# Optimization experiments

Measured on AMD Instinct MI355X. Metric: run time of the kernel, lower is better.

The kernel has to match this reference:

```python
import jax, jax.numpy as jnp
import numpy as np

B, LQ, LK, D = 4, 2048, 2048, 1024
H = 16  # num_heads == num_kv_heads (only runnable config of the source module)
HD = D // H  # 64


def setup_inputs() -> dict:
    key = jax.random.key(0)
    ks = jax.random.split(key, 4)
    std = 0.02
    return {
        "x": jax.random.normal(ks[0], (B, LQ, D), dtype=jnp.float32),
        "text_input": jax.random.normal(ks[1], (B, LK, D), dtype=jnp.float32),
        "Wq": jax.random.normal(ks[2], (D, D), dtype=jnp.float32) * std,
        "bq": jnp.zeros((D,), dtype=jnp.float32),
        "Wkv": jax.random.normal(ks[3], (D, 2 * D), dtype=jnp.float32) * std,
        "bkv": jnp.zeros((2 * D,), dtype=jnp.float32),
    }


def reference(x, text_input, Wq, bq, Wkv, bkv):
    b, lq, d = x.shape
    lk = text_input.shape[1]
    # projections
    Q = x @ Wq + bq                       # [b, lq, d]
    KV = text_input @ Wkv + bkv           # [b, lk, 2d]
    K, V = jnp.split(KV, 2, axis=-1)      # [b, lk, d] each
    # split heads (num_kv_heads == num_heads, so repeat_interleave is identity)
    Q = Q.reshape(b, lq, H, HD)
    K = K.reshape(b, lk, H, HD)
    V = V.reshape(b, lk, H, HD)
    # scaled dot-product attention
    scale = 1.0 / jnp.sqrt(jnp.asarray(HD, dtype=Q.dtype))
    scores = jnp.einsum("bqhd,bkhd->bhqk", Q, K) * scale  # [b, H, lq, lk]
    attn = jax.nn.softmax(scores, axis=-1)
    out = jnp.einsum("bhqk,bkhd->bqhd", attn, V)          # [b, lq, H, HD]
    # dropout p=0.0 (eval) -> identity
    return out.reshape(b, lq, d)
```

## Files before the change

### kernel.cpp

```cpp
#include <hip/hip_runtime.h>
#include <hip/hip_bf16.h>


typedef unsigned short u16;
typedef unsigned int u32;

typedef __attribute__((ext_vector_type(8))) __bf16 bf16x8;
typedef __attribute__((ext_vector_type(2))) _Float16 f16x2;
typedef __attribute__((ext_vector_type(8))) _Float16 f16x8;
typedef __attribute__((ext_vector_type(4))) float f32x4;
typedef __attribute__((ext_vector_type(4))) float f4;
typedef __attribute__((ext_vector_type(4))) unsigned short u16x4;

#define DEVI __device__ __forceinline__

DEVI u16 f2b(float f) {
  u32 u = __float_as_uint(f);
  return (u16)((u + 0x7fffu + ((u >> 16) & 1u)) >> 16);
}

DEVI u16 f2h(float f) {
  _Float16 h = (_Float16)f;
  return __builtin_bit_cast(u16, h);
}

DEVI f16x2 pk_f16(float a, float b) {
  return __builtin_bit_cast(f16x2, __builtin_amdgcn_cvt_pkrtz(a, b));
}

DEVI void gld_lds16(void* lds, const void* g) {
  __builtin_amdgcn_global_load_lds(
      (const __attribute__((address_space(1))) u32*)g,
      (__attribute__((address_space(3))) u32*)lds, 16, 0, 0);
}

__global__ __launch_bounds__(256) void k_prep(
    const float* __restrict__ x, const float* __restrict__ text,
    const float* __restrict__ Wq, const float* __restrict__ Wkv,
    u16* __restrict__ XB, u16* __restrict__ TB,
    u16* __restrict__ WQT, u16* __restrict__ WKVT) {
  __shared__ float tile[32][33];
  const int bid = blockIdx.x, tid = threadIdx.x;
  if (bid < 4096) {
    const float* in = (bid < 2048) ? x : text;
    u16* out = (bid < 2048) ? XB : TB;
    const int cb = (bid < 2048) ? bid : bid - 2048;
#pragma unroll
    for (int it = 0; it < 4; it++) {
      int i = cb * 256 + tid + it * 524288;
      f4 v = ((const f4*)in)[i];
      u16x4 o;
      o.x = f2b(v.x); o.y = f2b(v.y); o.z = f2b(v.z); o.w = f2b(v.w);
      ((u16x4*)out)[i] = o;
    }
  } else {
    const float* in;
    u16* out;
    int N, bx, by;
    if (bid < 5120) {
      int b2 = bid - 4096; in = Wq; out = WQT; N = 1024; bx = b2 & 31; by = b2 >> 5;
    } else {
      int b2 = bid - 5120; in = Wkv; out = WKVT; N = 2048; bx = b2 & 63; by = b2 >> 6;
    }
    const int K = 1024;
    const int n0 = bx * 32, k0 = by * 32;
    const int tx = tid & 31, ty = tid >> 5;
#pragma unroll
    for (int j = 0; j < 32; j += 8)
      tile[ty + j][tx] = in[(size_t)(k0 + ty + j) * N + n0 + tx];
    __syncthreads();
#pragma unroll
    for (int j = 0; j < 32; j += 8)
      out[(size_t)(n0 + ty + j) * K + k0 + tx] = f2b(tile[tx][ty + j]);
  }
}

__global__ __launch_bounds__(256) void k_gemm(
    const u16* __restrict__ XB, const u16* __restrict__ TB,
    const u16* __restrict__ WQT, const u16* __restrict__ WKVT,
    const float* __restrict__ bq, const float* __restrict__ bkv,
    u16* __restrict__ QG, u16* __restrict__ KG, u16* __restrict__ VG) {
  __shared__ alignas(16) char As[2][8192];
  __shared__ alignas(16) char Bs[2][8192];
  const int bid = blockIdx.x;
  const int tid = threadIdx.x;
  const int w = tid >> 6, l = tid & 63;
  const int wr = w >> 1, wc = w & 1;

  const bool isQ = bid < 512;
  int nb, mb;
  const u16 *Aptr, *Bptr;
  const float* bias;
  if (isQ) {
    nb = bid & 7; mb = bid >> 3; Aptr = XB; Bptr = WQT; bias = bq;
  } else {
    int b2 = bid - 512; nb = b2 & 15; mb = b2 >> 4; Aptr = TB; Bptr = WKVT; bias = bkv;
  }
  const int m0 = mb << 7, n0 = nb << 7;

  u32 soff[2], doff[2];
#pragma unroll
  for (int i = 0; i < 2; i++) {
    u32 o = (u32)(i * 4096 + tid * 16);
    u32 row = o >> 6;
    soff[i] = row * 2048 + ((o & 63) ^ ((row & 3) << 4));
    doff[i] = o;
  }
  const char* Aorig = (const char*)Aptr + (size_t)m0 * 2048;
  const char* Borig = (const char*)Bptr + (size_t)n0 * 2048;

  f32x4 acc[4][4];
#pragma unroll
  for (int i = 0; i < 4; i++)
#pragma unroll
    for (int j = 0; j < 4; j++) acc[i][j] = (f32x4){0.f, 0.f, 0.f, 0.f};

  const u32 co = (u32)(((l >> 4) ^ (l & 3)) << 4);
  const u32 arow = (u32)(wr * 64 + (l & 15)) * 64;
  const u32 brow = (u32)(wc * 64 + (l & 15)) * 64;

#pragma unroll
  for (int i = 0; i < 2; i++) {
    gld_lds16(&As[0][doff[i]], Aorig + soff[i]);
    gld_lds16(&Bs[0][doff[i]], Borig + soff[i]);
  }
  __syncthreads();
  int buf = 0;
  for (int kt = 0; kt < 32; kt++) {
    if (kt < 31) {
#pragma unroll
      for (int i = 0; i < 2; i++) {
        gld_lds16(&As[buf ^ 1][doff[i]], Aorig + (u32)(kt + 1) * 64 + soff[i]);
        gld_lds16(&Bs[buf ^ 1][doff[i]], Borig + (u32)(kt + 1) * 64 + soff[i]);
      }
    }
    bf16x8 af[4], bfr[4];
#pragma unroll
    for (int t = 0; t < 4; t++) {
      af[t] = *(const bf16x8*)&As[buf][arow + (u32)t * 1024 + co];
      bfr[t] = *(const bf16x8*)&Bs[buf][brow + (u32)t * 1024 + co];
    }
#pragma unroll
    for (int i = 0; i < 4; i++)
#pragma unroll
      for (int j = 0; j < 4; j++)
        acc[i][j] = __builtin_amdgcn_mfma_f32_16x16x32_bf16(af[i], bfr[j], acc[i][j], 0, 0, 0);
    __syncthreads();
    buf ^= 1;
  }

#pragma unroll
  for (int i = 0; i < 4; i++) {
    const int mbase = m0 + wr * 64 + i * 16 + ((l >> 4) << 2);
    const int bb = mbase >> 11;
    const int mrow = mbase & 2047;
#pragma unroll
    for (int j = 0; j < 4; j++) {
      const int n = n0 + wc * 64 + j * 16 + (l & 15);
      const float bv = bias[n];
      if (isQ) {
        const int h = n >> 6, hd = n & 63;
        u16* dst = QG + ((((size_t)bb * 16 + h) * 2048 + mrow) << 6) + hd;
#pragma unroll
        for (int r = 0; r < 4; r++)
          dst[(size_t)r << 6] = f2b((acc[i][j][r] + bv) * 0.18033688011112042f);
      } else if (n < 1024) {
        const int h = n >> 6, d = n & 63;
        char* base = (char*)KG + ((((size_t)bb * 16 + h) * 2048 + mrow) << 7);
#pragma unroll
        for (int r = 0; r < 4; r++) {
          u32 off = (u32)r * 128 + (((u32)d * 2) ^ (((u32)(mrow + r) & 7) << 4));
          *(u16*)(base + off) = f2b(acc[i][j][r] + bv);
        }
      } else {
        const int nn = n - 1024;
        const int h = nn >> 6, hd = nn & 63;
        u16x4 pk;
        pk.x = f2h(acc[i][j][0] + bv);
        pk.y = f2h(acc[i][j][1] + bv);
        pk.z = f2h(acc[i][j][2] + bv);
        pk.w = f2h(acc[i][j][3] + bv);
        char* base = (char*)VG + (((size_t)bb * 16 + h) << 18);
        u32 off = ((u32)(mrow >> 6) << 13) + (((u32)(mrow >> 5) & 1) << 12) +
                  ((u32)(hd >> 4) << 10) + (((u32)(mrow >> 2) & 3) << 8) +
                  ((u32)(hd & 15) << 4) + (((u32)(mrow >> 4) & 1) << 3);
        *(u16x4*)(base + off) = pk;
      }
    }
  }
}

__global__ __launch_bounds__(256) void k_attn(
    const u16* __restrict__ QG, const u16* __restrict__ KG, const u16* __restrict__ VG,
    float* __restrict__ out) {
  __shared__ alignas(16) char Ks[2][8192];
  __shared__ alignas(16) char Vs[2][8192];
  const int tid = threadIdx.x, w = tid >> 6, l = tid & 63;
  const int g = l >> 4, q = l & 15;
  const int bid = blockIdx.x;
  const int orig = (bid & 7) * 128 + (bid >> 3);
  const int qt = orig & 15;
  const int hh = (orig >> 4) & 15;
  const int b = orig >> 8;
  const size_t bh = (size_t)b * 16 + hh;

  const int qrowA = qt * 128 + w * 16 + q;
  const int qrowB = qrowA + 64;

  const u16* QpA = QG + ((bh * 2048 + (size_t)qrowA) << 6) + (g << 3);
  const u16* QpB = QG + ((bh * 2048 + (size_t)qrowB) << 6) + (g << 3);
  const bf16x8 qf0a = *(const bf16x8*)QpA;
  const bf16x8 qf1a = *(const bf16x8*)(QpA + 32);
  const bf16x8 qf0b = *(const bf16x8*)QpB;
  const bf16x8 qf1b = *(const bf16x8*)(QpB + 32);

  const char* Kbase = (const char*)KG + (bh << 18);
  const char* Vbase = (const char*)VG + (bh << 18);

  f32x4 lsA = (f32x4){0.f, 0.f, 0.f, 0.f};
  f32x4 lsB = (f32x4){0.f, 0.f, 0.f, 0.f};
  f32x4 oa[4], ob4[4];
#pragma unroll
  for (int c = 0; c < 4; c++) {
    oa[c] = (f32x4){0.f, 0.f, 0.f, 0.f};
    ob4[c] = (f32x4){0.f, 0.f, 0.f, 0.f};
  }
  f16x8 ones8;
#pragma unroll
  for (int e = 0; e < 8; e++) ones8[e] = (_Float16)1.0f;

  gld_lds16(&Ks[0][tid * 16], Kbase + tid * 16);
  gld_lds16(&Ks[0][4096 + tid * 16], Kbase + 4096 + tid * 16);
  gld_lds16(&Vs[0][tid * 16], Vbase + tid * 16);
  gld_lds16(&Vs[0][4096 + tid * 16], Vbase + 4096 + tid * 16);
  __syncthreads();

  const u32 ksw = ((u32)(l & 7)) << 4;
  const u32 kro = ((u32)q) << 7;
  const u32 kin = ((u32)g) << 4;

  auto body = [&](int BUF, int kb) {
    if (kb < 31) {
      const char* kp = Kbase + (size_t)(kb + 1) * 8192 + tid * 16;
      const char* vp = Vbase + (size_t)(kb + 1) * 8192 + tid * 16;
      gld_lds16(&Ks[BUF ^ 1][tid * 16], kp);
      gld_lds16(&Ks[BUF ^ 1][4096 + tid * 16], kp + 4096);
      gld_lds16(&Vs[BUF ^ 1][tid * 16], vp);
      gld_lds16(&Vs[BUF ^ 1][4096 + tid * 16], vp + 4096);
    }
    f32x4 sa[4], sb[4];
    __builtin_amdgcn_s_setprio(1);
#pragma unroll
    for (int t = 0; t < 4; t++) {
      const char* kr = &Ks[BUF][kro + (u32)t * 2048];
      bf16x8 kf0 = *(const bf16x8*)(kr + (kin ^ ksw));
      bf16x8 kf1 = *(const bf16x8*)(kr + ((kin + 64) ^ ksw));
      f32x4 z = (f32x4){0.f, 0.f, 0.f, 0.f};
      sa[t] = __builtin_amdgcn_mfma_f32_16x16x32_bf16(kf0, qf0a, z, 0, 0, 0);
      sa[t] = __builtin_amdgcn_mfma_f32_16x16x32_bf16(kf1, qf1a, sa[t], 0, 0, 0);
      sb[t] = __builtin_amdgcn_mfma_f32_16x16x32_bf16(kf0, qf0b, z, 0, 0, 0);
      sb[t] = __builtin_amdgcn_mfma_f32_16x16x32_bf16(kf1, qf1b, sb[t], 0, 0, 0);
    }
    __builtin_amdgcn_s_setprio(0);

    float pA[4][4], pB[4][4];
#pragma unroll
    for (int t = 0; t < 4; t++)
#pragma unroll
      for (int r = 0; r < 4; r++) {
        pA[t][r] = __builtin_amdgcn_exp2f(sa[t][r]);
        pB[t][r] = __builtin_amdgcn_exp2f(sb[t][r]);
      }

    __builtin_amdgcn_s_setprio(1);
#pragma unroll
    for (int u = 0; u < 2; u++) {
      f16x2 a0 = pk_f16(pA[2 * u][0], pA[2 * u][1]);
      f16x2 a1 = pk_f16(pA[2 * u][2], pA[2 * u][3]);
      f16x2 a2 = pk_f16(pA[2 * u + 1][0], pA[2 * u + 1][1]);
      f16x2 a3 = pk_f16(pA[2 * u + 1][2], pA[2 * u + 1][3]);
      f16x8 pfa;
      pfa[0] = a0.x; pfa[1] = a0.y; pfa[2] = a1.x; pfa[3] = a1.y;
      pfa[4] = a2.x; pfa[5] = a2.y; pfa[6] = a3.x; pfa[7] = a3.y;
      f16x2 b0 = pk_f16(pB[2 * u][0], pB[2 * u][1]);
      f16x2 b1 = pk_f16(pB[2 * u][2], pB[2 * u][3]);
      f16x2 b2 = pk_f16(pB[2 * u + 1][0], pB[2 * u + 1][1]);
      f16x2 b3 = pk_f16(pB[2 * u + 1][2], pB[2 * u + 1][3]);
      f16x8 pfb;
      pfb[0] = b0.x; pfb[1] = b0.y; pfb[2] = b1.x; pfb[3] = b1.y;
      pfb[4] = b2.x; pfb[5] = b2.y; pfb[6] = b3.x; pfb[7] = b3.y;
      lsA = __builtin_amdgcn_mfma_f32_16x16x32_f16(ones8, pfa, lsA, 0, 0, 0);
      lsB = __builtin_amdgcn_mfma_f32_16x16x32_f16(ones8, pfb, lsB, 0, 0, 0);
#pragma unroll
      for (int c = 0; c < 4; c++) {
        f16x8 vf = *(const f16x8*)&Vs[BUF][(u32)u * 4096 + (u32)c * 1024 + (u32)l * 16];
        oa[c] = __builtin_amdgcn_mfma_f32_16x16x32_f16(vf, pfa, oa[c], 0, 0, 0);
        ob4[c] = __builtin_amdgcn_mfma_f32_16x16x32_f16(vf, pfb, ob4[c], 0, 0, 0);
      }
    }
    __builtin_amdgcn_s_setprio(0);
    __syncthreads();
  };

  for (int kb2 = 0; kb2 < 16; kb2++) {
    body(0, 2 * kb2);
    body(1, 2 * kb2 + 1);
  }

  const float invA = 1.0f / lsA.x;
  const float invB = 1.0f / lsB.x;
  float* obA = out + ((size_t)b * 2048 + (size_t)qrowA) * 1024 + hh * 64;
  float* obB = out + ((size_t)b * 2048 + (size_t)qrowB) * 1024 + hh * 64;
#pragma unroll
  for (int c = 0; c < 4; c++) {
    f32x4 va = oa[c] * invA;
    f32x4 vb2 = ob4[c] * invB;
    *(f32x4*)(obA + c * 16 + g * 4) = va;
    *(f32x4*)(obB + c * 16 + g * 4) = vb2;
  }
}

extern "C" void kernel_launch(void* const* d_in, const int* in_sizes, int n_in,
                              void* d_out, int out_size, void* d_ws, size_t ws_size,
                              hipStream_t stream) {
  const float* x = (const float*)d_in[0];
  const float* text = (const float*)d_in[1];
  const float* Wq = (const float*)d_in[2];
  const float* bq = (const float*)d_in[3];
  const float* Wkv = (const float*)d_in[4];
  const float* bkv = (const float*)d_in[5];
  float* out = (float*)d_out;
  char* ws = (char*)d_ws;

  const size_t MiB = 1u << 20;
  u16* XB = (u16*)(ws + 0 * MiB);
  u16* TB = (u16*)(ws + 16 * MiB);
  u16* WQT = (u16*)(ws + 32 * MiB);
  u16* WKVT = (u16*)(ws + 34 * MiB);
  u16* QG = (u16*)(ws + 38 * MiB);
  u16* KG = (u16*)(ws + 54 * MiB);
  u16* VG = (u16*)(ws + 70 * MiB);

  k_prep<<<7168, 256, 0, stream>>>(x, text, Wq, Wkv, XB, TB, WQT, WKVT);
  k_gemm<<<1536, 256, 0, stream>>>(XB, TB, WQT, WKVT, bq, bkv, QG, KG, VG);
  k_attn<<<1024, 256, 0, stream>>>(QG, KG, VG, out);
}
```

Baseline: 181.7 us.

## Use 32x32 MFMA in projection GEMM and VALU row sums in attention

The projection GEMM moves from 16x16x32 to 32x32x16 bf16 MFMA tiles, with new LDS fragment indexing and an epilogue that matches the 32x32 accumulator layout. This cuts LDS fragment loads per MFMA and raises operand reuse. In attention, the softmax denominator is no longer computed with a ones-vector MFMA. Each lane now sums its exp values in fp32 registers and the partial sums are reduced with cross-lane shuffles at the end, which frees the matrix pipe but adds VALU adds and keeps the denominator in fp32 instead of the fp16-rounded values.

```diff
diff --git a/kernel.cpp b/kernel.cpp
--- a/kernel.cpp
+++ b/kernel.cpp
@@ -9,8 +9,10 @@
 typedef __attribute__((ext_vector_type(2))) _Float16 f16x2;
 typedef __attribute__((ext_vector_type(8))) _Float16 f16x8;
 typedef __attribute__((ext_vector_type(4))) float f32x4;
+typedef __attribute__((ext_vector_type(16))) float f32x16;
 typedef __attribute__((ext_vector_type(4))) float f4;
 typedef __attribute__((ext_vector_type(4))) unsigned short u16x4;
+typedef __attribute__((ext_vector_type(4))) unsigned int u32x4;
 
 #define DEVI __device__ __forceinline__
 
@@ -24,8 +26,8 @@
   return __builtin_bit_cast(u16, h);
 }
 
-DEVI f16x2 pk_f16(float a, float b) {
-  return __builtin_bit_cast(f16x2, __builtin_amdgcn_cvt_pkrtz(a, b));
+DEVI u32 pk_f16u(float a, float b) {
+  return __builtin_bit_cast(u32, __builtin_amdgcn_cvt_pkrtz(a, b));
 }
 
 DEVI void gld_lds16(void* lds, const void* g) {
@@ -109,15 +111,18 @@
   const char* Aorig = (const char*)Aptr + (size_t)m0 * 2048;
   const char* Borig = (const char*)Bptr + (size_t)n0 * 2048;
 
-  f32x4 acc[4][4];
-#pragma unroll
-  for (int i = 0; i < 4; i++)
-#pragma unroll
-    for (int j = 0; j < 4; j++) acc[i][j] = (f32x4){0.f, 0.f, 0.f, 0.f};
-
-  const u32 co = (u32)(((l >> 4) ^ (l & 3)) << 4);
-  const u32 arow = (u32)(wr * 64 + (l & 15)) * 64;
-  const u32 brow = (u32)(wc * 64 + (l & 15)) * 64;
+  f32x16 acc[2][2];
+#pragma unroll
+  for (int i = 0; i < 2; i++)
+#pragma unroll
+    for (int j = 0; j < 2; j++)
+#pragma unroll
+      for (int e = 0; e < 16; e++) acc[i][j][e] = 0.f;
+
+  const u32 x3 = (u32)(l & 3);
+  const u32 hi5 = (u32)(l >> 5);
+  const u32 arow0 = (u32)(wr * 64 + (l & 31)) * 64;
+  const u32 brow0 = (u32)(wc * 64 + (l & 31)) * 64;
 
 #pragma unroll
   for (int i = 0; i < 2; i++) {
@@ -134,60 +139,70 @@
         gld_lds16(&Bs[buf ^ 1][doff[i]], Borig + (u32)(kt + 1) * 64 + soff[i]);
       }
     }
-    bf16x8 af[4], bfr[4];
-#pragma unroll
-    for (int t = 0; t < 4; t++) {
-      af[t] = *(const bf16x8*)&As[buf][arow + (u32)t * 1024 + co];
-      bfr[t] = *(const bf16x8*)&Bs[buf][brow + (u32)t * 1024 + co];
-    }
-#pragma unroll
-    for (int i = 0; i < 4; i++)
-#pragma unroll
-      for (int j = 0; j < 4; j++)
-        acc[i][j] = __builtin_amdgcn_mfma_f32_16x16x32_bf16(af[i], bfr[j], acc[i][j], 0, 0, 0);
+    bf16x8 af[2][2], bfr[2][2];
+#pragma unroll
+    for (int i = 0; i < 2; i++)
+#pragma unroll
+      for (int h = 0; h < 2; h++) {
+        const u32 co = (((u32)(2 * h) + hi5) ^ x3) << 4;
+        af[i][h] = *(const bf16x8*)&As[buf][arow0 + (u32)i * 2048 + co];
+        bfr[i][h] = *(const bf16x8*)&Bs[buf][brow0 + (u32)i * 2048 + co];
+      }
+#pragma unroll
+    for (int i = 0; i < 2; i++)
+#pragma unroll
+      for (int j = 0; j < 2; j++)
+#pragma unroll
+        for (int h = 0; h < 2; h++)
+          acc[i][j] = __builtin_amdgcn_mfma_f32_32x32x16_bf16(af[i][h], bfr[j][h], acc[i][j], 0, 0, 0);
     __syncthreads();
     buf ^= 1;
   }
 
 #pragma unroll
-  for (int i = 0; i < 4; i++) {
-    const int mbase = m0 + wr * 64 + i * 16 + ((l >> 4) << 2);
-    const int bb = mbase >> 11;
-    const int mrow = mbase & 2047;
-#pragma unroll
-    for (int j = 0; j < 4; j++) {
-      const int n = n0 + wc * 64 + j * 16 + (l & 15);
+  for (int i = 0; i < 2; i++)
+#pragma unroll
+    for (int j = 0; j < 2; j++) {
+      const int n = n0 + wc * 64 + j * 32 + (l & 31);
       const float bv = bias[n];
-      if (isQ) {
-        const int h = n >> 6, hd = n & 63;
-        u16* dst = QG + ((((size_t)bb * 16 + h) * 2048 + mrow) << 6) + hd;
-#pragma unroll
-        for (int r = 0; r < 4; r++)
-          dst[(size_t)r << 6] = f2b((acc[i][j][r] + bv) * 0.18033688011112042f);
-      } else if (n < 1024) {
-        const int h = n >> 6, d = n & 63;
-        char* base = (char*)KG + ((((size_t)bb * 16 + h) * 2048 + mrow) << 7);
-#pragma unroll
-        for (int r = 0; r < 4; r++) {
-          u32 off = (u32)r * 128 + (((u32)d * 2) ^ (((u32)(mrow + r) & 7) << 4));
-          *(u16*)(base + off) = f2b(acc[i][j][r] + bv);
+#pragma unroll
+      for (int rg = 0; rg < 4; rg++) {
+        const int mbase = m0 + wr * 64 + i * 32 + rg * 8 + ((l >> 5) << 2);
+        const int bb = mbase >> 11;
+        const int mrow = mbase & 2047;
+        float a0 = acc[i][j][rg * 4 + 0] + bv;
+        float a1 = acc[i][j][rg * 4 + 1] + bv;
+        float a2 = acc[i][j][rg * 4 + 2] + bv;
+        float a3 = acc[i][j][rg * 4 + 3] + bv;
+        if (isQ) {
+          const int h = n >> 6, hd = n & 63;
+          u16* dst = QG + ((((size_t)bb * 16 + h) * 2048 + mrow) << 6) + hd;
+          dst[0] = f2b(a0 * 0.18033688011112042f);
+          dst[64] = f2b(a1 * 0.18033688011112042f);
+          dst[128] = f2b(a2 * 0.18033688011112042f);
+          dst[192] = f2b(a3 * 0.18033688011112042f);
+        } else if (n < 1024) {
+          const int h = n >> 6, d = n & 63;
+          char* base = (char*)KG + ((((size_t)bb * 16 + h) * 2048 + mrow) << 7);
+          float av[4] = {a0, a1, a2, a3};
+#pragma unroll
+          for (int r = 0; r < 4; r++) {
+            u32 off = (u32)r * 128 + (((u32)d * 2) ^ (((u32)(mrow + r) & 7) << 4));
+            *(u16*)(base + off) = f2b(av[r]);
+          }
+        } else {
+          const int nn = n - 1024;
+          const int h = nn >> 6, hd = nn & 63;
+          u16x4 pk;
+          pk.x = f2h(a0); pk.y = f2h(a1); pk.z = f2h(a2); pk.w = f2h(a3);
+          char* base = (char*)VG + (((size_t)bb * 16 + h) << 18);
+          u32 off = ((u32)(mrow >> 6) << 13) + (((u32)(mrow >> 5) & 1) << 12) +
+                    ((u32)(hd >> 4) << 10) + (((u32)(mrow >> 2) & 3) << 8) +
+                    ((u32)(hd & 15) << 4) + (((u32)(mrow >> 4) & 1) << 3);
+          *(u16x4*)(base + off) = pk;
         }
-      } else {
-        const int nn = n - 1024;
-        const int h = nn >> 6, hd = nn & 63;
-        u16x4 pk;
-        pk.x = f2h(acc[i][j][0] + bv);
-        pk.y = f2h(acc[i][j][1] + bv);
-        pk.z = f2h(acc[i][j][2] + bv);
-        pk.w = f2h(acc[i][j][3] + bv);
-        char* base = (char*)VG + (((size_t)bb * 16 + h) << 18);
-        u32 off = ((u32)(mrow >> 6) << 13) + (((u32)(mrow >> 5) & 1) << 12) +
-                  ((u32)(hd >> 4) << 10) + (((u32)(mrow >> 2) & 3) << 8) +
-                  ((u32)(hd & 15) << 4) + (((u32)(mrow >> 4) & 1) << 3);
-        *(u16x4*)(base + off) = pk;
-      }
-    }
-  }
+      }
+    }
 }
 
 __global__ __launch_bounds__(256) void k_attn(
@@ -217,17 +232,13 @@
   const char* Kbase = (const char*)KG + (bh << 18);
   const char* Vbase = (const char*)VG + (bh << 18);
 
-  f32x4 lsA = (f32x4){0.f, 0.f, 0.f, 0.f};
-  f32x4 lsB = (f32x4){0.f, 0.f, 0.f, 0.f};
+  float ls_a0 = 0.f, ls_a1 = 0.f, ls_b0 = 0.f, ls_b1 = 0.f;
   f32x4 oa[4], ob4[4];
 #pragma unroll
   for (int c = 0; c < 4; c++) {
     oa[c] = (f32x4){0.f, 0.f, 0.f, 0.f};
     ob4[c] = (f32x4){0.f, 0.f, 0.f, 0.f};
   }
-  f16x8 ones8;
-#pragma unroll
-  for (int e = 0; e < 8; e++) ones8[e] = (_Float16)1.0f;
 
   gld_lds16(&Ks[0][tid * 16], Kbase + tid * 16);
   gld_lds16(&Ks[0][4096 + tid * 16], Kbase + 4096 + tid * 16);
@@ -270,27 +281,24 @@
       for (int r = 0; r < 4; r++) {
         pA[t][r] = __builtin_amdgcn_exp2f(sa[t][r]);
         pB[t][r] = __builtin_amdgcn_exp2f(sb[t][r]);
+        if (r & 1) { ls_a1 += pA[t][r]; ls_b1 += pB[t][r]; }
+        else       { ls_a0 += pA[t][r]; ls_b0 += pB[t][r]; }
       }
 
     __builtin_amdgcn_s_setprio(1);
 #pragma unroll
     for (int u = 0; u < 2; u++) {
-      f16x2 a0 = pk_f16(pA[2 * u][0], pA[2 * u][1]);
-      f16x2 a1 = pk_f16(pA[2 * u][2], pA[2 * u][3]);
-      f16x2 a2 = pk_f16(pA[2 * u + 1][0], pA[2 * u + 1][1]);
-      f16x2 a3 = pk_f16(pA[2 * u + 1][2], pA[2 * u + 1][3]);
-      f16x8 pfa;
-      pfa[0] = a0.x; pfa[1] = a0.y; pfa[2] = a1.x; pfa[3] = a1.y;
-      pfa[4] = a2.x; pfa[5] = a2.y; pfa[6] = a3.x; pfa[7] = a3.y;
-      f16x2 b0 = pk_f16(pB[2 * u][0], pB[2 * u][1]);
-      f16x2 b1 = pk_f16(pB[2 * u][2], pB[2 * u][3]);
-      f16x2 b2 = pk_f16(pB[2 * u + 1][0], pB[2 * u + 1][1]);
-      f16x2 b3 = pk_f16(pB[2 * u + 1][2], pB[2 * u + 1][3]);
-      f16x8 pfb;
-      pfb[0] = b0.x; pfb[1] = b0.y; pfb[2] = b1.x; pfb[3] = b1.y;
-      pfb[4] = b2.x; pfb[5] = b2.y; pfb[6] = b3.x; pfb[7] = b3.y;
-      lsA = __builtin_amdgcn_mfma_f32_16x16x32_f16(ones8, pfa, lsA, 0, 0, 0);
-      lsB = __builtin_amdgcn_mfma_f32_16x16x32_f16(ones8, pfb, lsB, 0, 0, 0);
+      u32x4 ta, tb;
+      ta.x = pk_f16u(pA[2 * u][0], pA[2 * u][1]);
+      ta.y = pk_f16u(pA[2 * u][2], pA[2 * u][3]);
+      ta.z = pk_f16u(pA[2 * u + 1][0], pA[2 * u + 1][1]);
+      ta.w = pk_f16u(pA[2 * u + 1][2], pA[2 * u + 1][3]);
+      tb.x = pk_f16u(pB[2 * u][0], pB[2 * u][1]);
+      tb.y = pk_f16u(pB[2 * u][2], pB[2 * u][3]);
+      tb.z = pk_f16u(pB[2 * u + 1][0], pB[2 * u + 1][1]);
+      tb.w = pk_f16u(pB[2 * u + 1][2], pB[2 * u + 1][3]);
+      f16x8 pfa = __builtin_bit_cast(f16x8, ta);
+      f16x8 pfb = __builtin_bit_cast(f16x8, tb);
 #pragma unroll
       for (int c = 0; c < 4; c++) {
         f16x8 vf = *(const f16x8*)&Vs[BUF][(u32)u * 4096 + (u32)c * 1024 + (u32)l * 16];
@@ -307,8 +315,14 @@
     body(1, 2 * kb2 + 1);
   }
 
-  const float invA = 1.0f / lsA.x;
-  const float invB = 1.0f / lsB.x;
+  float lsa = ls_a0 + ls_a1;
+  float lsb = ls_b0 + ls_b1;
+  lsa += __shfl_xor(lsa, 16);
+  lsa += __shfl_xor(lsa, 32);
+  lsb += __shfl_xor(lsb, 16);
+  lsb += __shfl_xor(lsb, 32);
+  const float invA = 1.0f / lsa;
+  const float invB = 1.0f / lsb;
   float* obA = out + ((size_t)b * 2048 + (size_t)qrowA) * 1024 + hh * 64;
   float* obB = out + ((size_t)b * 2048 + (size_t)qrowB) * 1024 + hh * 64;
 #pragma unroll
```

Result: no change. 183.8 us (+1.1%).
